# Optimization experiments

Hardware: AMD Instinct MI355X
Metric: run time of the kernel (lower is better)

The kernel has to match this reference:

```python
import jax, jax.numpy as jnp
import numpy as np

N_NODES = 100000
N_EDGES = 1250000
F_RAW = 48      # raw node feature dim
F_LOC = 16      # location embedding dim
F1 = 48         # filters_1
F_OUT = 64      # out_channels


def _glorot(key, shape):
    fan_in, fan_out = shape[0], shape[1]
    scale = jnp.sqrt(6.0 / (fan_in + fan_out)).astype(jnp.float32)
    return jax.random.uniform(key, shape, jnp.float32, -1.0, 1.0) * scale


def setup_inputs() -> dict:
    key = jax.random.key(0)
    k_e, k_x, k_l, k_w1, k_w2 = jax.random.split(key, 5)
    edge_indices = jax.random.randint(k_e, (2, N_EDGES), 0, N_NODES, dtype=jnp.int64)
    features = jax.random.normal(k_x, (N_NODES, F_RAW), jnp.float32)
    location_embedding = jax.random.normal(k_l, (N_NODES, F_LOC), jnp.float32)
    W1 = _glorot(k_w1, (F_RAW + F_LOC, F1))
    b1 = jnp.zeros((F1,), jnp.float32)
    W2 = _glorot(k_w2, (F1 + F_LOC, F_OUT))
    b2 = jnp.zeros((F_OUT,), jnp.float32)
    return {"edge_indices": edge_indices, "features": features,
            "location_embedding": location_embedding,
            "W1": W1, "b1": b1, "W2": W2, "b2": b2}


def gcn_conv(x, src, dst, W, b, n_nodes):
    """PyG GCNConv: add self-loops, symmetric normalization, linear + bias."""
    h = x @ W  # [N, F_out]
    # degree counts include the self-loop (+1)
    deg = jnp.zeros((n_nodes,), h.dtype).at[dst].add(1.0) + 1.0
    dinv = jax.lax.rsqrt(deg)  # deg >= 1 so always finite
    coef = dinv[src] * dinv[dst]  # [E]
    agg = jnp.zeros((n_nodes, h.shape[1]), h.dtype).at[dst].add(h[src] * coef[:, None])
    # self-loop contribution: dinv[i]^2 * h[i]
    return agg + h * (dinv * dinv)[:, None] + b


def reference(edge_indices, features, location_embedding, W1, b1, W2, b2):
    src, dst = edge_indices[0], edge_indices[1]
    n = features.shape[0]
    x = jnp.concatenate([features, location_embedding], axis=-1)
    x = gcn_conv(x, src, dst, W1, b1, n)
    x = jax.nn.relu(x)
    # dropout is identity in eval mode (reference is inference semantics)
    x = jnp.concatenate([x, location_embedding], axis=-1)
    x = gcn_conv(x, src, dst, W2, b2, n)
    return x
```

## Files before the change

kernel.cpp:

```cpp
#include <hip/hip_runtime.h>
#include <hip/hip_fp16.h>

#define N_NODES 100000
#define N_EDGES 1250000
#define F_RAW 48
#define F_LOC 16
#define F1 48
#define F_IN1 64
#define F_IN2 64
#define F_OUT 64

#define NB_BIN 100
#define CHUNK (N_EDGES / NB_BIN)
#define NBUK 391
#define NSCAN (NBUK * NB_BIN)
#define NSCAN_PARTS ((NSCAN + 1023) / 1024)

typedef _Float16 half8_t __attribute__((ext_vector_type(8)));
typedef float floatx4 __attribute__((ext_vector_type(4)));

__global__ void k_detect(const unsigned* edges_u32, int* flag) {
    __shared__ int any;
    if (threadIdx.x == 0) any = 0;
    __syncthreads();
    int nz = 0;
    for (int i = threadIdx.x; i < 2048; i += 256) {
        if (edges_u32[2 * i + 1] != 0u) nz = 1;
    }
    if (nz) atomicOr(&any, 1);
    __syncthreads();
    if (threadIdx.x == 0) *flag = any;
}

__device__ __forceinline__ void load_edge(const void* edges, int is32, int e,
                                          int& s, int& d) {
    if (is32) {
        const int* p = (const int*)edges;
        s = p[e];
        d = p[N_EDGES + e];
    } else {
        const long long* p = (const long long*)edges;
        s = (int)p[e];
        d = (int)p[N_EDGES + e];
    }
}

__global__ __launch_bounds__(1024) void k_prepA(const void* edges,
                                                const int* flag,
                                                int* __restrict__ src32,
                                                int* __restrict__ dst32,
                                                int* __restrict__ bhist) {
    __shared__ int hist[NBUK];
    int b = blockIdx.x, t = threadIdx.x;
    for (int k = t; k < NBUK; k += 1024) hist[k] = 0;
    __syncthreads();
    int is32 = *flag;
    int e0 = b * CHUNK;
    int e1 = e0 + CHUNK;
    for (int e = e0 + t; e < e1; e += 1024) {
        int s, d;
        load_edge(edges, is32, e, s, d);
        src32[e] = s;
        dst32[e] = d;
        atomicAdd(&hist[d >> 8], 1);
    }
    __syncthreads();
    for (int k = t; k < NBUK; k += 1024) bhist[k * NB_BIN + b] = hist[k];
}

__global__ __launch_bounds__(256) void k_gscan_part(const int* __restrict__ in,
                                                    int* __restrict__ part,
                                                    int n) {
    int b = blockIdx.x, t = threadIdx.x;
    int i0 = b * 1024 + t * 4;
    int s = 0;
#pragma unroll
    for (int j = 0; j < 4; ++j) {
        int i = i0 + j;
        if (i < n) s += in[i];
    }
#pragma unroll
    for (int m = 1; m < 64; m <<= 1) s += __shfl_xor(s, m);
    __shared__ int ws[4];
    if ((t & 63) == 0) ws[t >> 6] = s;
    __syncthreads();
    if (t == 0) part[b] = ws[0] + ws[1] + ws[2] + ws[3];
}

__global__ __launch_bounds__(64) void k_gscan_top(int* __restrict__ part,
                                                  int nb) {
    int t = threadIdx.x;
    int v = (t < nb) ? part[t] : 0;
    int x = v;
#pragma unroll
    for (int off = 1; off < 64; off <<= 1) {
        int u = __shfl_up(x, off);
        if (t >= off) x += u;
    }
    if (t < nb) part[t] = x - v;
}

__global__ __launch_bounds__(256) void k_gscan_down(int* __restrict__ data,
                                                    const int* __restrict__ part,
                                                    int n) {
    int b = blockIdx.x, t = threadIdx.x;
    int lane = t & 63, wv = t >> 6;
    int i0 = b * 1024 + t * 4;
    int v[4];
    int s = 0;
#pragma unroll
    for (int j = 0; j < 4; ++j) {
        int i = i0 + j;
        v[j] = (i < n) ? data[i] : 0;
        s += v[j];
    }
    int x = s;
#pragma unroll
    for (int off = 1; off < 64; off <<= 1) {
        int u = __shfl_up(x, off);
        if (lane >= off) x += u;
    }
    __shared__ int ws[4];
    if (lane == 63) ws[wv] = x;
    __syncthreads();
    int woff = 0;
    for (int w = 0; w < wv; ++w) woff += ws[w];
    int run = part[b] + woff + (x - s);
#pragma unroll
    for (int j = 0; j < 4; ++j) {
        int i = i0 + j;
        if (i < n) {
            data[i] = run;
            run += v[j];
        }
    }
}

__global__ __launch_bounds__(1024) void k_place(const int* __restrict__ src32,
                                                const int* __restrict__ dst32,
                                                const int* __restrict__ bhist,
                                                unsigned* __restrict__ binned) {
    __shared__ int cnt[NBUK];
    int b = blockIdx.x, t = threadIdx.x;
    for (int k = t; k < NBUK; k += 1024) cnt[k] = bhist[k * NB_BIN + b];
    __syncthreads();
    int e0 = b * CHUNK;
    int e1 = e0 + CHUNK;
    for (int e = e0 + t; e < e1; e += 1024) {
        int s = src32[e];
        int d = dst32[e];
        int p = atomicAdd(&cnt[d >> 8], 1);
        binned[p] = ((unsigned)(d & 255) << 17) | (unsigned)s;
    }
}

__global__ __launch_bounds__(256) void k_bucket(
    const unsigned* __restrict__ binned, const int* __restrict__ bhist,
    float* __restrict__ dinv, int* __restrict__ rowptr,
    unsigned* __restrict__ csr4) {
    int k = blockIdx.x, t = threadIdx.x;
    int lane = t & 63, wv = t >> 6;
    __shared__ int ldeg[256];
    __shared__ int wcnt[256];
    __shared__ int ws4[4];
    int base = bhist[k * NB_BIN];
    int next = (k + 1 < NBUK) ? bhist[(k + 1) * NB_BIN] : N_EDGES;
    int len = next - base;
    ldeg[t] = 0;
    __syncthreads();
    for (int i = t; i < len; i += 256)
        atomicAdd(&ldeg[binned[base + i] >> 17], 1);
    __syncthreads();
    int degv = ldeg[t];
    int x = degv;
#pragma unroll
    for (int off = 1; off < 64; off <<= 1) {
        int u = __shfl_up(x, off);
        if (lane >= off) x += u;
    }
    if (lane == 63) ws4[wv] = x;
    __syncthreads();
    int woff = 0;
    for (int w = 0; w < wv; ++w) woff += ws4[w];
    int excl = woff + x - degv;
    int node = k * 256 + t;
    if (node < N_NODES) {
        dinv[node] = rsqrtf((float)degv + 1.0f);
        rowptr[node] = base + excl;
    }
    wcnt[t] = base + excl;
    __syncthreads();
    for (int i = t; i < len; i += 256) {
        unsigned ent = binned[base + i];
        int dl = ent >> 17;
        int p = atomicAdd(&wcnt[dl], 1);
        csr4[p] = ent & 0x1FFFFu;
    }
    if (k == 0 && t == 0) rowptr[N_NODES] = N_EDGES;
}

__global__ __launch_bounds__(256) void k_csr8(const unsigned* __restrict__ csr4,
                                              const float* __restrict__ dinv,
                                              int2* __restrict__ csr8) {
    int i = blockIdx.x * 256 + threadIdx.x;
    if (i >= N_EDGES / 2) return;
    uint2 v = reinterpret_cast<const uint2*>(csr4)[i];
    unsigned h0 = (unsigned)__half_as_ushort(__float2half(dinv[v.x]));
    unsigned h1 = (unsigned)__half_as_ushort(__float2half(dinv[v.y]));
    int4 o;
    o.x = (int)(v.x << 7);
    o.y = (int)(h0 | (h0 << 16));
    o.z = (int)(v.y << 7);
    o.w = (int)(h1 | (h1 << 16));
    reinterpret_cast<int4*>(csr8)[i] = o;
}

__global__ void k_wprep(const float* __restrict__ W, __half* __restrict__ Wpk,
                        int M, int CT) {
    int lane = threadIdx.x;
    for (int ct = 0; ct < CT; ++ct)
        for (int kt = 0; kt < 2; ++kt)
            for (int j = 0; j < 8; ++j) {
                int k = kt * 32 + (lane >> 4) * 8 + j;
                int c = ct * 16 + (lane & 15);
                Wpk[((ct * 2 + kt) * 64 + lane) * 8 + j] =
                    __float2half(W[k * M + c]);
            }
}

__global__ __launch_bounds__(256) void k_gemm1(const float* __restrict__ feat,
                                               const float* __restrict__ loc,
                                               const __half* __restrict__ Wpk,
                                               __half* __restrict__ Y) {
    int wid = threadIdx.x >> 6;
    int lane = threadIdx.x & 63;
    int nb = (blockIdx.x * 4 + wid) * 32;
    if (nb >= N_NODES) return;
    half8_t b[3][2];
#pragma unroll
    for (int ct = 0; ct < 3; ++ct)
#pragma unroll
        for (int kt = 0; kt < 2; ++kt)
            b[ct][kt] = *reinterpret_cast<const half8_t*>(
                Wpk + ((ct * 2 + kt) * 64 + lane) * 8);
    int r = lane & 15;
    int slot = lane >> 4;
    half8_t a[2][2];
#pragma unroll
    for (int rt = 0; rt < 2; ++rt)
#pragma unroll
        for (int kt = 0; kt < 2; ++kt) {
            int sl = kt * 4 + slot;
            int node = nb + rt * 16 + r;
            const float* sp = (sl < 6)
                                  ? feat + (size_t)node * F_RAW + sl * 8
                                  : loc + (size_t)node * F_LOC + (sl - 6) * 8;
            float4 f0 = reinterpret_cast<const float4*>(sp)[0];
            float4 f1 = reinterpret_cast<const float4*>(sp)[1];
            half8_t h;
            h[0] = (_Float16)f0.x;
            h[1] = (_Float16)f0.y;
            h[2] = (_Float16)f0.z;
            h[3] = (_Float16)f0.w;
            h[4] = (_Float16)f1.x;
            h[5] = (_Float16)f1.y;
            h[6] = (_Float16)f1.z;
            h[7] = (_Float16)f1.w;
            a[rt][kt] = h;
        }
    floatx4 acc[2][3];
#pragma unroll
    for (int rt = 0; rt < 2; ++rt)
#pragma unroll
        for (int ct = 0; ct < 3; ++ct) {
            floatx4 z = {0.f, 0.f, 0.f, 0.f};
            z = __builtin_amdgcn_mfma_f32_16x16x32_f16(a[rt][0], b[ct][0], z, 0, 0, 0);
            z = __builtin_amdgcn_mfma_f32_16x16x32_f16(a[rt][1], b[ct][1], z, 0, 0, 0);
            acc[rt][ct] = z;
        }
    int row0 = (lane >> 4) * 4;
    int col = lane & 15;
#pragma unroll
    for (int rt = 0; rt < 2; ++rt)
#pragma unroll
        for (int ct = 0; ct < 3; ++ct)
#pragma unroll
            for (int j = 0; j < 4; ++j) {
                int node = nb + rt * 16 + row0 + j;
                Y[(size_t)node * 64 + ct * 16 + col] = __float2half(acc[rt][ct][j]);
            }
    int node = nb + (lane & 31);
    int slotp = 6 + (lane >> 5);
    *reinterpret_cast<int4*>(Y + (size_t)node * 64 + slotp * 8) =
        make_int4(0, 0, 0, 0);
}

__global__ __launch_bounds__(256) void k_gemm2(const __half* __restrict__ X,
                                               const __half* __restrict__ Wpk,
                                               __half* __restrict__ Y) {
    int wid = threadIdx.x >> 6;
    int lane = threadIdx.x & 63;
    int nb = (blockIdx.x * 4 + wid) * 32;
    if (nb >= N_NODES) return;
    half8_t b[4][2];
#pragma unroll
    for (int ct = 0; ct < 4; ++ct)
#pragma unroll
        for (int kt = 0; kt < 2; ++kt)
            b[ct][kt] = *reinterpret_cast<const half8_t*>(
                Wpk + ((ct * 2 + kt) * 64 + lane) * 8);
    int r = lane & 15;
    int ks = (lane >> 4) * 8;
    half8_t a[2][2];
#pragma unroll
    for (int rt = 0; rt < 2; ++rt)
#pragma unroll
        for (int kt = 0; kt < 2; ++kt)
            a[rt][kt] = *reinterpret_cast<const half8_t*>(
                X + ((size_t)(nb + rt * 16 + r) * 64 + kt * 32 + ks));
    floatx4 acc[2][4];
#pragma unroll
    for (int rt = 0; rt < 2; ++rt)
#pragma unroll
        for (int ct = 0; ct < 4; ++ct) {
            floatx4 z = {0.f, 0.f, 0.f, 0.f};
            z = __builtin_amdgcn_mfma_f32_16x16x32_f16(a[rt][0], b[ct][0], z, 0, 0, 0);
            z = __builtin_amdgcn_mfma_f32_16x16x32_f16(a[rt][1], b[ct][1], z, 0, 0, 0);
            acc[rt][ct] = z;
        }
    int row0 = (lane >> 4) * 4;
    int col = lane & 15;
#pragma unroll
    for (int rt = 0; rt < 2; ++rt)
#pragma unroll
        for (int ct = 0; ct < 4; ++ct)
#pragma unroll
            for (int j = 0; j < 4; ++j) {
                int node = nb + rt * 16 + row0 + j;
                Y[(size_t)node * 64 + ct * 16 + col] = __float2half(acc[rt][ct][j]);
            }
}

__device__ __forceinline__ __half2 h2bits(int y) {
    return *reinterpret_cast<__half2*>(&y);
}

__device__ __forceinline__ void fma8h(const int4& p, __half2 c2, __half2 a[4]) {
    const __half2* h = reinterpret_cast<const __half2*>(&p);
#pragma unroll
    for (int j = 0; j < 4; ++j) a[j] = __hfma2(h[j], c2, a[j]);
}

__device__ __forceinline__ __half2 shfl_xor_h2(__half2 v, int m) {
    int i = *reinterpret_cast<int*>(&v);
    i = __shfl_xor(i, m);
    return *reinterpret_cast<__half2*>(&i);
}

__global__ __launch_bounds__(256) void k_agg1(
    const __half* __restrict__ h1h, const float* __restrict__ dinv,
    const int* __restrict__ rowptr, const int2* __restrict__ csr8,
    const float* __restrict__ loc, const float* __restrict__ b1,
    __half* __restrict__ x1h) {
    int wave = threadIdx.x >> 6;
    int lane = threadIdx.x & 63;
    int grp = lane >> 3;
    int l8 = lane & 7;
    int node = blockIdx.x * 4 + wave;
    if (node >= N_NODES) return;
    int r0 = rowptr[node], r1 = rowptr[node + 1];
    const char* h1l = reinterpret_cast<const char*>(h1h) + (l8 << 4);
    float di = dinv[node];
    int4 hs = *reinterpret_cast<const int4*>(h1l + ((size_t)node << 7));
    int len = r1 - r0;
    int L = (len + 7) >> 3;
    int gs = r0 + grp * L;
    int ge = gs + L;
    if (ge > r1) ge = r1;
    __half2 z2 = __float2half2_rn(0.f);
    __half2 a0[4] = {z2, z2, z2, z2};
    __half2 a1[4] = {z2, z2, z2, z2};
    int e = gs;
    for (; e + 1 < ge; e += 2) {
        int2 A = csr8[e];
        int2 B = csr8[e + 1];
        int4 vA = *reinterpret_cast<const int4*>(h1l + A.x);
        int4 vB = *reinterpret_cast<const int4*>(h1l + B.x);
        fma8h(vA, h2bits(A.y), a0);
        fma8h(vB, h2bits(B.y), a1);
    }
    if (e < ge) {
        int2 A = csr8[e];
        int4 vA = *reinterpret_cast<const int4*>(h1l + A.x);
        fma8h(vA, h2bits(A.y), a0);
    }
#pragma unroll
    for (int j = 0; j < 4; ++j) a0[j] = __hadd2(a0[j], a1[j]);
#pragma unroll
    for (int j = 0; j < 4; ++j) {
        a0[j] = __hadd2(a0[j], shfl_xor_h2(a0[j], 8));
        a0[j] = __hadd2(a0[j], shfl_xor_h2(a0[j], 16));
        a0[j] = __hadd2(a0[j], shfl_xor_h2(a0[j], 32));
    }
    if (lane < 8) {
        __half2 q[4];
        if (l8 < 6) {
            float d2 = di * di;
            const float4* b1v = reinterpret_cast<const float4*>(b1);
            float4 bA = b1v[l8 * 2];
            float4 bB = b1v[l8 * 2 + 1];
            float bb[8] = {bA.x, bA.y, bA.z, bA.w, bB.x, bB.y, bB.z, bB.w};
            const __half2* hh = reinterpret_cast<const __half2*>(&hs);
            float o[8];
#pragma unroll
            for (int j = 0; j < 4; ++j) {
                float2 t = __half22float2(hh[j]);
                float2 ag = __half22float2(a0[j]);
                o[2 * j] = fmaxf(fmaf(ag.x, di, fmaf(t.x, d2, bb[2 * j])), 0.f);
                o[2 * j + 1] =
                    fmaxf(fmaf(ag.y, di, fmaf(t.y, d2, bb[2 * j + 1])), 0.f);
            }
#pragma unroll
            for (int j = 0; j < 4; ++j)
                q[j] = __halves2half2(__float2half(o[2 * j]),
                                      __float2half(o[2 * j + 1]));
        } else {
            const float* lp = loc + (size_t)node * F_LOC + (l8 - 6) * 8;
            float4 f0 = reinterpret_cast<const float4*>(lp)[0];
            float4 f1 = reinterpret_cast<const float4*>(lp)[1];
            q[0] = __halves2half2(__float2half(f0.x), __float2half(f0.y));
            q[1] = __halves2half2(__float2half(f0.z), __float2half(f0.w));
            q[2] = __halves2half2(__float2half(f1.x), __float2half(f1.y));
            q[3] = __halves2half2(__float2half(f1.z), __float2half(f1.w));
        }
        reinterpret_cast<int4*>(x1h)[(size_t)node * 8 + l8] =
            *reinterpret_cast<int4*>(q);
    }
}

__global__ __launch_bounds__(256) void k_out(
    const __half* __restrict__ h2h, const float* __restrict__ dinv,
    const int* __restrict__ rowptr, const int2* __restrict__ csr8,
    const float* __restrict__ b2, float* __restrict__ out) {
    int wave = threadIdx.x >> 6;
    int lane = threadIdx.x & 63;
    int grp = lane >> 3;
    int l8 = lane & 7;
    int node = blockIdx.x * 4 + wave;
    if (node >= N_NODES) return;
    int r0 = rowptr[node], r1 = rowptr[node + 1];
    const char* h2l = reinterpret_cast<const char*>(h2h) + (l8 << 4);
    float di = dinv[node];
    int4 hs = *reinterpret_cast<const int4*>(h2l + ((size_t)node << 7));
    int len = r1 - r0;
    int L = (len + 7) >> 3;
    int gs = r0 + grp * L;
    int ge = gs + L;
    if (ge > r1) ge = r1;
    __half2 z2 = __float2half2_rn(0.f);
    __half2 a0[4] = {z2, z2, z2, z2};
    __half2 a1[4] = {z2, z2, z2, z2};
    int e = gs;
    for (; e + 1 < ge; e += 2) {
        int2 A = csr8[e];
        int2 B = csr8[e + 1];
        int4 vA = *reinterpret_cast<const int4*>(h2l + A.x);
        int4 vB = *reinterpret_cast<const int4*>(h2l + B.x);
        fma8h(vA, h2bits(A.y), a0);
        fma8h(vB, h2bits(B.y), a1);
    }
    if (e < ge) {
        int2 A = csr8[e];
        int4 vA = *reinterpret_cast<const int4*>(h2l + A.x);
        fma8h(vA, h2bits(A.y), a0);
    }
#pragma unroll
    for (int j = 0; j < 4; ++j) a0[j] = __hadd2(a0[j], a1[j]);
#pragma unroll
    for (int j = 0; j < 4; ++j) {
        a0[j] = __hadd2(a0[j], shfl_xor_h2(a0[j], 8));
        a0[j] = __hadd2(a0[j], shfl_xor_h2(a0[j], 16));
        a0[j] = __hadd2(a0[j], shfl_xor_h2(a0[j], 32));
    }
    if (lane < 8) {
        float d2 = di * di;
        const float4* b2v = reinterpret_cast<const float4*>(b2);
        float4 bA = b2v[l8 * 2];
        float4 bB = b2v[l8 * 2 + 1];
        float bb[8] = {bA.x, bA.y, bA.z, bA.w, bB.x, bB.y, bB.z, bB.w};
        const __half2* hh = reinterpret_cast<const __half2*>(&hs);
        float o[8];
#pragma unroll
        for (int j = 0; j < 4; ++j) {
            float2 t = __half22float2(hh[j]);
            float2 ag = __half22float2(a0[j]);
            o[2 * j] = fmaf(ag.x, di, fmaf(t.x, d2, bb[2 * j]));
            o[2 * j + 1] = fmaf(ag.y, di, fmaf(t.y, d2, bb[2 * j + 1]));
        }
        float4* ov = reinterpret_cast<float4*>(out + (size_t)node * F_OUT);
        ov[l8 * 2] = make_float4(o[0], o[1], o[2], o[3]);
        ov[l8 * 2 + 1] = make_float4(o[4], o[5], o[6], o[7]);
    }
}

extern "C" void kernel_launch(void* const* d_in, const int* in_sizes, int n_in,
                              void* d_out, int out_size, void* d_ws,
                              size_t ws_size, hipStream_t stream) {
    const void* edges = d_in[0];
    const float* feat = (const float*)d_in[1];
    const float* loc = (const float*)d_in[2];
    const float* W1 = (const float*)d_in[3];
    const float* b1 = (const float*)d_in[4];
    const float* W2 = (const float*)d_in[5];
    const float* b2 = (const float*)d_in[6];
    float* out = (float*)d_out;

    char* ws = (char*)d_ws;
    float* dinv = (float*)(ws + 0);
    int* rowptr = (int*)(ws + 400000);
    int* src32 = (int*)(ws + 800016);
    int* dst32 = (int*)(ws + 5800016);
    int* bhist = (int*)(ws + 10800016);
    int* bsum = (int*)(ws + 10956416);
    unsigned* binned = (unsigned*)(ws + 10956672);
    unsigned* csr4 = (unsigned*)(ws + 15956672);
    __half* x1h = (__half*)(ws + 20956672);
    __half* h1h = (__half*)(ws + 33756672);
    __half* h2h = (__half*)(ws + 46556672);
    __half* wpk1 = (__half*)(ws + 59356672);
    __half* wpk2 = (__half*)(ws + 59362816);
    int* flag = (int*)(ws + 59371008);
    int2* csr8 = (int2*)(ws + 800016);

    k_detect<<<1, 256, 0, stream>>>((const unsigned*)edges, flag);
    k_wprep<<<1, 64, 0, stream>>>(W1, wpk1, F1, 3);
    k_wprep<<<1, 64, 0, stream>>>(W2, wpk2, F_OUT, 4);

    k_prepA<<<NB_BIN, 1024, 0, stream>>>(edges, flag, src32, dst32, bhist);
    k_gscan_part<<<NSCAN_PARTS, 256, 0, stream>>>(bhist, bsum, NSCAN);
    k_gscan_top<<<1, 64, 0, stream>>>(bsum, NSCAN_PARTS);
    k_gscan_down<<<NSCAN_PARTS, 256, 0, stream>>>(bhist, bsum, NSCAN);
    k_place<<<NB_BIN, 1024, 0, stream>>>(src32, dst32, bhist, binned);
    k_bucket<<<NBUK, 256, 0, stream>>>(binned, bhist, dinv, rowptr, csr4);
    k_csr8<<<(N_EDGES / 2 + 255) / 256, 256, 0, stream>>>(csr4, dinv, csr8);

    int gblocks = (N_NODES / 32 + 3) / 4;
    k_gemm1<<<gblocks, 256, 0, stream>>>(feat, loc, wpk1, h1h);
    k_agg1<<<(N_NODES + 3) / 4, 256, 0, stream>>>(h1h, dinv, rowptr, csr8,
                                                  loc, b1, x1h);
    k_gemm2<<<gblocks, 256, 0, stream>>>(x1h, wpk2, h2h);
    k_out<<<(N_NODES + 3) / 4, 256, 0, stream>>>(h2h, dinv, rowptr, csr8, b2,
                                                 out);
}
```

Baseline: 165.4 us.

## Split transformed features into column slabs and pack coefficient into CSR word

The GEMM outputs are stored as separate 32-column and 16/32-column slabs instead of one padded 64-half row. The aggregation kernels gather each slab in a separate pass over the edge list, so each pass reads a smaller, more cache-resident table. The per-edge coefficient is now packed into the low 14 bits of a 4-byte CSR entry, which halves index traffic compared with the previous 8-byte entries. The three tiny prep kernels are merged into one launch. In exchange, the edge list is read twice, the coefficient keeps only 14 bits of the fp16 value (dropping the sign bit, which is safe because it is always positive), and an extra shuffle step is needed to reassemble the outputs.

```diff
diff --git a/kernel.cpp b/kernel.cpp
--- a/kernel.cpp
+++ b/kernel.cpp
@@ -6,8 +6,6 @@
 #define F_RAW 48
 #define F_LOC 16
 #define F1 48
-#define F_IN1 64
-#define F_IN2 64
 #define F_OUT 64
 
 #define NB_BIN 100
@@ -19,7 +17,30 @@
 typedef _Float16 half8_t __attribute__((ext_vector_type(8)));
 typedef float floatx4 __attribute__((ext_vector_type(4)));
 
-__global__ void k_detect(const unsigned* edges_u32, int* flag) {
+__device__ void wprep_dev(const float* W, __half* Wpk, int M, int CT) {
+    int lane = threadIdx.x;
+    if (lane >= 64) return;
+    for (int ct = 0; ct < CT; ++ct)
+        for (int kt = 0; kt < 2; ++kt)
+            for (int j = 0; j < 8; ++j) {
+                int k = kt * 32 + (lane >> 4) * 8 + j;
+                int c = ct * 16 + (lane & 15);
+                Wpk[((ct * 2 + kt) * 64 + lane) * 8 + j] =
+                    __float2half(W[k * M + c]);
+            }
+}
+
+__global__ void k_misc(const unsigned* edges_u32, int* flag,
+                       const float* W1, __half* wpk1,
+                       const float* W2, __half* wpk2) {
+    if (blockIdx.x == 1) {
+        wprep_dev(W1, wpk1, F1, 3);
+        return;
+    }
+    if (blockIdx.x == 2) {
+        wprep_dev(W2, wpk2, F_OUT, 4);
+        return;
+    }
     __shared__ int any;
     if (threadIdx.x == 0) any = 0;
     __syncthreads();
@@ -199,39 +220,23 @@
     if (k == 0 && t == 0) rowptr[N_NODES] = N_EDGES;
 }
 
-__global__ __launch_bounds__(256) void k_csr8(const unsigned* __restrict__ csr4,
-                                              const float* __restrict__ dinv,
-                                              int2* __restrict__ csr8) {
+__global__ __launch_bounds__(256) void k_coef(unsigned* __restrict__ csr4,
+                                              const float* __restrict__ dinv) {
     int i = blockIdx.x * 256 + threadIdx.x;
-    if (i >= N_EDGES / 2) return;
-    uint2 v = reinterpret_cast<const uint2*>(csr4)[i];
-    unsigned h0 = (unsigned)__half_as_ushort(__float2half(dinv[v.x]));
-    unsigned h1 = (unsigned)__half_as_ushort(__float2half(dinv[v.y]));
-    int4 o;
-    o.x = (int)(v.x << 7);
-    o.y = (int)(h0 | (h0 << 16));
-    o.z = (int)(v.y << 7);
-    o.w = (int)(h1 | (h1 << 16));
-    reinterpret_cast<int4*>(csr8)[i] = o;
-}
-
-__global__ void k_wprep(const float* __restrict__ W, __half* __restrict__ Wpk,
-                        int M, int CT) {
-    int lane = threadIdx.x;
-    for (int ct = 0; ct < CT; ++ct)
-        for (int kt = 0; kt < 2; ++kt)
-            for (int j = 0; j < 8; ++j) {
-                int k = kt * 32 + (lane >> 4) * 8 + j;
-                int c = ct * 16 + (lane & 15);
-                Wpk[((ct * 2 + kt) * 64 + lane) * 8 + j] =
-                    __float2half(W[k * M + c]);
-            }
+    if (i >= N_EDGES / 4) return;
+    uint4 v = reinterpret_cast<uint4*>(csr4)[i];
+    v.x = (v.x << 14) | (unsigned)__half_as_ushort(__float2half(dinv[v.x]));
+    v.y = (v.y << 14) | (unsigned)__half_as_ushort(__float2half(dinv[v.y]));
+    v.z = (v.z << 14) | (unsigned)__half_as_ushort(__float2half(dinv[v.z]));
+    v.w = (v.w << 14) | (unsigned)__half_as_ushort(__float2half(dinv[v.w]));
+    reinterpret_cast<uint4*>(csr4)[i] = v;
 }
 
 __global__ __launch_bounds__(256) void k_gemm1(const float* __restrict__ feat,
                                                const float* __restrict__ loc,
                                                const __half* __restrict__ Wpk,
-                                               __half* __restrict__ Y) {
+                                               __half* __restrict__ h1a,
+                                               __half* __restrict__ h1b) {
     int wid = threadIdx.x >> 6;
     int lane = threadIdx.x & 63;
     int nb = (blockIdx.x * 4 + wid) * 32;
@@ -287,17 +292,18 @@
 #pragma unroll
             for (int j = 0; j < 4; ++j) {
                 int node = nb + rt * 16 + row0 + j;
-                Y[(size_t)node * 64 + ct * 16 + col] = __float2half(acc[rt][ct][j]);
+                if (ct < 2)
+                    h1a[(size_t)node * 32 + ct * 16 + col] =
+                        __float2half(acc[rt][ct][j]);
+                else
+                    h1b[(size_t)node * 16 + col] = __float2half(acc[rt][ct][j]);
             }
-    int node = nb + (lane & 31);
-    int slotp = 6 + (lane >> 5);
-    *reinterpret_cast<int4*>(Y + (size_t)node * 64 + slotp * 8) =
-        make_int4(0, 0, 0, 0);
 }
 
 __global__ __launch_bounds__(256) void k_gemm2(const __half* __restrict__ X,
                                                const __half* __restrict__ Wpk,
-                                               __half* __restrict__ Y) {
+                                               __half* __restrict__ h2a,
+                                               __half* __restrict__ h2b) {
     int wid = threadIdx.x >> 6;
     int lane = threadIdx.x & 63;
     int nb = (blockIdx.x * 4 + wid) * 32;
@@ -337,7 +343,12 @@
 #pragma unroll
             for (int j = 0; j < 4; ++j) {
                 int node = nb + rt * 16 + row0 + j;
-                Y[(size_t)node * 64 + ct * 16 + col] = __float2half(acc[rt][ct][j]);
+                if (ct < 2)
+                    h2a[(size_t)node * 32 + ct * 16 + col] =
+                        __float2half(acc[rt][ct][j]);
+                else
+                    h2b[(size_t)node * 32 + (ct - 2) * 16 + col] =
+                        __float2half(acc[rt][ct][j]);
             }
 }
 
@@ -345,23 +356,26 @@
     return *reinterpret_cast<__half2*>(&y);
 }
 
-__device__ __forceinline__ void fma8h(const int4& p, __half2 c2, __half2 a[4]) {
-    const __half2* h = reinterpret_cast<const __half2*>(&p);
-#pragma unroll
-    for (int j = 0; j < 4; ++j) a[j] = __hfma2(h[j], c2, a[j]);
+__device__ __forceinline__ int as_int_h2(__half2 v) {
+    return *reinterpret_cast<int*>(&v);
+}
+
+__device__ __forceinline__ __half2 coef2(unsigned A) {
+    unsigned b = A & 0x3FFFu;
+    return h2bits((int)(b | (b << 16)));
 }
 
 __device__ __forceinline__ __half2 shfl_xor_h2(__half2 v, int m) {
-    int i = *reinterpret_cast<int*>(&v);
+    int i = as_int_h2(v);
     i = __shfl_xor(i, m);
-    return *reinterpret_cast<__half2*>(&i);
+    return h2bits(i);
 }
 
 __global__ __launch_bounds__(256) void k_agg1(
-    const __half* __restrict__ h1h, const float* __restrict__ dinv,
-    const int* __restrict__ rowptr, const int2* __restrict__ csr8,
-    const float* __restrict__ loc, const float* __restrict__ b1,
-    __half* __restrict__ x1h) {
+    const __half* __restrict__ h1a, const __half* __restrict__ h1b,
+    const float* __restrict__ dinv, const int* __restrict__ rowptr,
+    const unsigned* __restrict__ csr4, const float* __restrict__ loc,
+    const float* __restrict__ b1, __half* __restrict__ x1h) {
     int wave = threadIdx.x >> 6;
     int lane = threadIdx.x & 63;
     int grp = lane >> 3;
@@ -369,63 +383,99 @@
     int node = blockIdx.x * 4 + wave;
     if (node >= N_NODES) return;
     int r0 = rowptr[node], r1 = rowptr[node + 1];
-    const char* h1l = reinterpret_cast<const char*>(h1h) + (l8 << 4);
-    float di = dinv[node];
-    int4 hs = *reinterpret_cast<const int4*>(h1l + ((size_t)node << 7));
     int len = r1 - r0;
     int L = (len + 7) >> 3;
     int gs = r0 + grp * L;
     int ge = gs + L;
     if (ge > r1) ge = r1;
+    float di = dinv[node];
+    const char* pa = reinterpret_cast<const char*>(h1a) + l8 * 8;
+    const char* pb = reinterpret_cast<const char*>(h1b) + l8 * 4;
     __half2 z2 = __float2half2_rn(0.f);
-    __half2 a0[4] = {z2, z2, z2, z2};
-    __half2 a1[4] = {z2, z2, z2, z2};
+    __half2 a0[2] = {z2, z2}, a1[2] = {z2, z2};
     int e = gs;
     for (; e + 1 < ge; e += 2) {
-        int2 A = csr8[e];
-        int2 B = csr8[e + 1];
-        int4 vA = *reinterpret_cast<const int4*>(h1l + A.x);
-        int4 vB = *reinterpret_cast<const int4*>(h1l + B.x);
-        fma8h(vA, h2bits(A.y), a0);
-        fma8h(vB, h2bits(B.y), a1);
+        unsigned A = csr4[e];
+        unsigned B = csr4[e + 1];
+        int2 vA = *reinterpret_cast<const int2*>(pa + ((A >> 14) << 6));
+        int2 vB = *reinterpret_cast<const int2*>(pa + ((B >> 14) << 6));
+        __half2 cA = coef2(A), cB = coef2(B);
+        a0[0] = __hfma2(h2bits(vA.x), cA, a0[0]);
+        a0[1] = __hfma2(h2bits(vA.y), cA, a0[1]);
+        a1[0] = __hfma2(h2bits(vB.x), cB, a1[0]);
+        a1[1] = __hfma2(h2bits(vB.y), cB, a1[1]);
     }
     if (e < ge) {
-        int2 A = csr8[e];
-        int4 vA = *reinterpret_cast<const int4*>(h1l + A.x);
-        fma8h(vA, h2bits(A.y), a0);
-    }
-#pragma unroll
-    for (int j = 0; j < 4; ++j) a0[j] = __hadd2(a0[j], a1[j]);
-#pragma unroll
-    for (int j = 0; j < 4; ++j) {
-        a0[j] = __hadd2(a0[j], shfl_xor_h2(a0[j], 8));
-        a0[j] = __hadd2(a0[j], shfl_xor_h2(a0[j], 16));
-        a0[j] = __hadd2(a0[j], shfl_xor_h2(a0[j], 32));
+        unsigned A = csr4[e];
+        int2 vA = *reinterpret_cast<const int2*>(pa + ((A >> 14) << 6));
+        __half2 cA = coef2(A);
+        a0[0] = __hfma2(h2bits(vA.x), cA, a0[0]);
+        a0[1] = __hfma2(h2bits(vA.y), cA, a0[1]);
+    }
+    a0[0] = __hadd2(a0[0], a1[0]);
+    a0[1] = __hadd2(a0[1], a1[1]);
+    __half2 b0 = z2, b1c = z2;
+    e = gs;
+    for (; e + 1 < ge; e += 2) {
+        unsigned A = csr4[e];
+        unsigned B = csr4[e + 1];
+        int vA = *reinterpret_cast<const int*>(pb + ((A >> 14) << 5));
+        int vB = *reinterpret_cast<const int*>(pb + ((B >> 14) << 5));
+        b0 = __hfma2(h2bits(vA), coef2(A), b0);
+        b1c = __hfma2(h2bits(vB), coef2(B), b1c);
+    }
+    if (e < ge) {
+        unsigned A = csr4[e];
+        int vA = *reinterpret_cast<const int*>(pb + ((A >> 14) << 5));
+        b0 = __hfma2(h2bits(vA), coef2(A), b0);
+    }
+    b0 = __hadd2(b0, b1c);
+#pragma unroll
+    for (int m = 8; m <= 32; m <<= 1) {
+        a0[0] = __hadd2(a0[0], shfl_xor_h2(a0[0], m));
+        a0[1] = __hadd2(a0[1], shfl_xor_h2(a0[1], m));
+        b0 = __hadd2(b0, shfl_xor_h2(b0, m));
+    }
+    int ai0 = as_int_h2(a0[0]), ai1 = as_int_h2(a0[1]), bi = as_int_h2(b0);
+    int m = l8;
+    int s0 = (m < 4) ? 2 * m : (m - 4) * 4;
+    int t00 = __shfl(ai0, s0), t01 = __shfl(ai1, s0);
+    int t10 = __shfl(ai0, s0 + 1), t11 = __shfl(ai1, s0 + 1);
+    int u0 = __shfl(bi, s0), u1 = __shfl(bi, s0 + 1);
+    int u2 = __shfl(bi, s0 + 2), u3 = __shfl(bi, s0 + 3);
+    int w[4];
+    if (m < 4) {
+        w[0] = t00; w[1] = t01; w[2] = t10; w[3] = t11;
+    } else {
+        w[0] = u0; w[1] = u1; w[2] = u2; w[3] = u3;
     }
     if (lane < 8) {
         __half2 q[4];
-        if (l8 < 6) {
+        if (m < 6) {
             float d2 = di * di;
             const float4* b1v = reinterpret_cast<const float4*>(b1);
-            float4 bA = b1v[l8 * 2];
-            float4 bB = b1v[l8 * 2 + 1];
+            float4 bA = b1v[m * 2];
+            float4 bB = b1v[m * 2 + 1];
             float bb[8] = {bA.x, bA.y, bA.z, bA.w, bB.x, bB.y, bB.z, bB.w};
+            int4 hs = (m < 4)
+                          ? *reinterpret_cast<const int4*>(
+                                reinterpret_cast<const char*>(h1a) +
+                                ((size_t)node << 6) + m * 16)
+                          : *reinterpret_cast<const int4*>(
+                                reinterpret_cast<const char*>(h1b) +
+                                ((size_t)node << 5) + (m - 4) * 16);
             const __half2* hh = reinterpret_cast<const __half2*>(&hs);
-            float o[8];
 #pragma unroll
             for (int j = 0; j < 4; ++j) {
                 float2 t = __half22float2(hh[j]);
-                float2 ag = __half22float2(a0[j]);
-                o[2 * j] = fmaxf(fmaf(ag.x, di, fmaf(t.x, d2, bb[2 * j])), 0.f);
-                o[2 * j + 1] =
+                float2 ag = __half22float2(h2bits(w[j]));
+                float o0 = fmaxf(fmaf(ag.x, di, fmaf(t.x, d2, bb[2 * j])), 0.f);
+                float o1 =
                     fmaxf(fmaf(ag.y, di, fmaf(t.y, d2, bb[2 * j + 1])), 0.f);
+                q[j] = __halves2half2(__float2half(o0), __float2half(o1));
             }
-#pragma unroll
-            for (int j = 0; j < 4; ++j)
-                q[j] = __halves2half2(__float2half(o[2 * j]),
-                                      __float2half(o[2 * j + 1]));
         } else {
-            const float* lp = loc + (size_t)node * F_LOC + (l8 - 6) * 8;
+            const float* lp = loc + (size_t)node * F_LOC + (m - 6) * 8;
             float4 f0 = reinterpret_cast<const float4*>(lp)[0];
             float4 f1 = reinterpret_cast<const float4*>(lp)[1];
             q[0] = __halves2half2(__float2half(f0.x), __float2half(f0.y));
@@ -433,15 +483,16 @@
             q[2] = __halves2half2(__float2half(f1.x), __float2half(f1.y));
             q[3] = __halves2half2(__float2half(f1.z), __float2half(f1.w));
         }
-        reinterpret_cast<int4*>(x1h)[(size_t)node * 8 + l8] =
+        reinterpret_cast<int4*>(x1h)[(size_t)node * 8 + m] =
             *reinterpret_cast<int4*>(q);
     }
 }
 
 __global__ __launch_bounds__(256) void k_out(
-    const __half* __restrict__ h2h, const float* __restrict__ dinv,
-    const int* __restrict__ rowptr, const int2* __restrict__ csr8,
-    const float* __restrict__ b2, float* __restrict__ out) {
+    const __half* __restrict__ h2a, const __half* __restrict__ h2b,
+    const float* __restrict__ dinv, const int* __restrict__ rowptr,
+    const unsigned* __restrict__ csr4, const float* __restrict__ b2,
+    float* __restrict__ out) {
     int wave = threadIdx.x >> 6;
     int lane = threadIdx.x & 63;
     int grp = lane >> 3;
@@ -449,57 +500,104 @@
     int node = blockIdx.x * 4 + wave;
     if (node >= N_NODES) return;
     int r0 = rowptr[node], r1 = rowptr[node + 1];
-    const char* h2l = reinterpret_cast<const char*>(h2h) + (l8 << 4);
-    float di = dinv[node];
-    int4 hs = *reinterpret_cast<const int4*>(h2l + ((size_t)node << 7));
     int len = r1 - r0;
     int L = (len + 7) >> 3;
     int gs = r0 + grp * L;
     int ge = gs + L;
     if (ge > r1) ge = r1;
+    float di = dinv[node];
+    const char* pa = reinterpret_cast<const char*>(h2a) + l8 * 8;
+    const char* pb = reinterpret_cast<const char*>(h2b) + l8 * 8;
     __half2 z2 = __float2half2_rn(0.f);
-    __half2 a0[4] = {z2, z2, z2, z2};
-    __half2 a1[4] = {z2, z2, z2, z2};
+    __half2 a0[2] = {z2, z2}, a1[2] = {z2, z2};
     int e = gs;
     for (; e + 1 < ge; e += 2) {
-        int2 A = csr8[e];
-        int2 B = csr8[e + 1];
-        int4 vA = *reinterpret_cast<const int4*>(h2l + A.x);
-        int4 vB = *reinterpret_cast<const int4*>(h2l + B.x);
-        fma8h(vA, h2bits(A.y), a0);
-        fma8h(vB, h2bits(B.y), a1);
+        unsigned A = csr4[e];
+        unsigned B = csr4[e + 1];
+        int2 vA = *reinterpret_cast<const int2*>(pa + ((A >> 14) << 6));
+        int2 vB = *reinterpret_cast<const int2*>(pa + ((B >> 14) << 6));
+        __half2 cA = coef2(A), cB = coef2(B);
+        a0[0] = __hfma2(h2bits(vA.x), cA, a0[0]);
+        a0[1] = __hfma2(h2bits(vA.y), cA, a0[1]);
+        a1[0] = __hfma2(h2bits(vB.x), cB, a1[0]);
+        a1[1] = __hfma2(h2bits(vB.y), cB, a1[1]);
     }
     if (e < ge) {
-        int2 A = csr8[e];
-        int4 vA = *reinterpret_cast<const int4*>(h2l + A.x);
-        fma8h(vA, h2bits(A.y), a0);
-    }
-#pragma unroll
-    for (int j = 0; j < 4; ++j) a0[j] = __hadd2(a0[j], a1[j]);
-#pragma unroll
-    for (int j = 0; j < 4; ++j) {
-        a0[j] = __hadd2(a0[j], shfl_xor_h2(a0[j], 8));
-        a0[j] = __hadd2(a0[j], shfl_xor_h2(a0[j], 16));
-        a0[j] = __hadd2(a0[j], shfl_xor_h2(a0[j], 32));
+        unsigned A = csr4[e];
+        int2 vA = *reinterpret_cast<const int2*>(pa + ((A >> 14) << 6));
+        __half2 cA = coef2(A);
+        a0[0] = __hfma2(h2bits(vA.x), cA, a0[0]);
+        a0[1] = __hfma2(h2bits(vA.y), cA, a0[1]);
+    }
+    a0[0] = __hadd2(a0[0], a1[0]);
+    a0[1] = __hadd2(a0[1], a1[1]);
+    __half2 c0[2] = {z2, z2}, c1[2] = {z2, z2};
+    e = gs;
+    for (; e + 1 < ge; e += 2) {
+        unsigned A = csr4[e];
+        unsigned B = csr4[e + 1];
+        int2 vA = *reinterpret_cast<const int2*>(pb + ((A >> 14) << 6));
+        int2 vB = *reinterpret_cast<const int2*>(pb + ((B >> 14) << 6));
+        __half2 cA = coef2(A), cB = coef2(B);
+        c0[0] = __hfma2(h2bits(vA.x), cA, c0[0]);
+        c0[1] = __hfma2(h2bits(vA.y), cA, c0[1]);
+        c1[0] = __hfma2(h2bits(vB.x), cB, c1[0]);
+        c1[1] = __hfma2(h2bits(vB.y), cB, c1[1]);
+    }
+    if (e < ge) {
+        unsigned A = csr4[e];
+        int2 vA = *reinterpret_cast<const int2*>(pb + ((A >> 14) << 6));
+        __half2 cA = coef2(A);
+        c0[0] = __hfma2(h2bits(vA.x), cA, c0[0]);
+        c0[1] = __hfma2(h2bits(vA.y), cA, c0[1]);
+    }
+    c0[0] = __hadd2(c0[0], c1[0]);
+    c0[1] = __hadd2(c0[1], c1[1]);
+#pragma unroll
+    for (int m = 8; m <= 32; m <<= 1) {
+        a0[0] = __hadd2(a0[0], shfl_xor_h2(a0[0], m));
+        a0[1] = __hadd2(a0[1], shfl_xor_h2(a0[1], m));
+        c0[0] = __hadd2(c0[0], shfl_xor_h2(c0[0], m));
+        c0[1] = __hadd2(c0[1], shfl_xor_h2(c0[1], m));
+    }
+    int ai0 = as_int_h2(a0[0]), ai1 = as_int_h2(a0[1]);
+    int bi0 = as_int_h2(c0[0]), bi1 = as_int_h2(c0[1]);
+    int m = l8;
+    int s0 = 2 * (m & 3);
+    int tA0 = __shfl(ai0, s0), tA1 = __shfl(ai1, s0);
+    int tA2 = __shfl(ai0, s0 + 1), tA3 = __shfl(ai1, s0 + 1);
+    int tB0 = __shfl(bi0, s0), tB1 = __shfl(bi1, s0);
+    int tB2 = __shfl(bi0, s0 + 1), tB3 = __shfl(bi1, s0 + 1);
+    int w[4];
+    if (m < 4) {
+        w[0] = tA0; w[1] = tA1; w[2] = tA2; w[3] = tA3;
+    } else {
+        w[0] = tB0; w[1] = tB1; w[2] = tB2; w[3] = tB3;
     }
     if (lane < 8) {
         float d2 = di * di;
         const float4* b2v = reinterpret_cast<const float4*>(b2);
-        float4 bA = b2v[l8 * 2];
-        float4 bB = b2v[l8 * 2 + 1];
+        float4 bA = b2v[m * 2];
+        float4 bB = b2v[m * 2 + 1];
         float bb[8] = {bA.x, bA.y, bA.z, bA.w, bB.x, bB.y, bB.z, bB.w};
+        int4 hs = (m < 4) ? *reinterpret_cast<const int4*>(
+                                reinterpret_cast<const char*>(h2a) +
+                                ((size_t)node << 6) + m * 16)
+                          : *reinterpret_cast<const int4*>(
+                                reinterpret_cast<const char*>(h2b) +
+                                ((size_t)node << 6) + (m - 4) * 16);
         const __half2* hh = reinterpret_cast<const __half2*>(&hs);
         float o[8];
 #pragma unroll
         for (int j = 0; j < 4; ++j) {
             float2 t = __half22float2(hh[j]);
-            float2 ag = __half22float2(a0[j]);
+            float2 ag = __half22float2(h2bits(w[j]));
             o[2 * j] = fmaf(ag.x, di, fmaf(t.x, d2, bb[2 * j]));
             o[2 * j + 1] = fmaf(ag.y, di, fmaf(t.y, d2, bb[2 * j + 1]));
         }
         float4* ov = reinterpret_cast<float4*>(out + (size_t)node * F_OUT);
-        ov[l8 * 2] = make_float4(o[0], o[1], o[2], o[3]);
-        ov[l8 * 2 + 1] = make_float4(o[4], o[5], o[6], o[7]);
+        ov[m * 2] = make_float4(o[0], o[1], o[2], o[3]);
+        ov[m * 2 + 1] = make_float4(o[4], o[5], o[6], o[7]);
     }
 }
 
@@ -525,16 +623,16 @@
     unsigned* binned = (unsigned*)(ws + 10956672);
     unsigned* csr4 = (unsigned*)(ws + 15956672);
     __half* x1h = (__half*)(ws + 20956672);
-    __half* h1h = (__half*)(ws + 33756672);
-    __half* h2h = (__half*)(ws + 46556672);
-    __half* wpk1 = (__half*)(ws + 59356672);
-    __half* wpk2 = (__half*)(ws + 59362816);
-    int* flag = (int*)(ws + 59371008);
-    int2* csr8 = (int2*)(ws + 800016);
-
-    k_detect<<<1, 256, 0, stream>>>((const unsigned*)edges, flag);
-    k_wprep<<<1, 64, 0, stream>>>(W1, wpk1, F1, 3);
-    k_wprep<<<1, 64, 0, stream>>>(W2, wpk2, F_OUT, 4);
+    __half* h1a = (__half*)(ws + 33756672);
+    __half* h1b = (__half*)(ws + 40156672);
+    __half* h2a = (__half*)(ws + 43356672);
+    __half* h2b = (__half*)(ws + 49756672);
+    __half* wpk1 = (__half*)(ws + 56156672);
+    __half* wpk2 = (__half*)(ws + 56162816);
+    int* flag = (int*)(ws + 56171008);
+
+    k_misc<<<3, 256, 0, stream>>>((const unsigned*)edges, flag, W1, wpk1, W2,
+                                  wpk2);
 
     k_prepA<<<NB_BIN, 1024, 0, stream>>>(edges, flag, src32, dst32, bhist);
     k_gscan_part<<<NSCAN_PARTS, 256, 0, stream>>>(bhist, bsum, NSCAN);
@@ -542,13 +640,13 @@
     k_gscan_down<<<NSCAN_PARTS, 256, 0, stream>>>(bhist, bsum, NSCAN);
     k_place<<<NB_BIN, 1024, 0, stream>>>(src32, dst32, bhist, binned);
     k_bucket<<<NBUK, 256, 0, stream>>>(binned, bhist, dinv, rowptr, csr4);
-    k_csr8<<<(N_EDGES / 2 + 255) / 256, 256, 0, stream>>>(csr4, dinv, csr8);
+    k_coef<<<(N_EDGES / 4 + 255) / 256, 256, 0, stream>>>(csr4, dinv);
 
     int gblocks = (N_NODES / 32 + 3) / 4;
-    k_gemm1<<<gblocks, 256, 0, stream>>>(feat, loc, wpk1, h1h);
-    k_agg1<<<(N_NODES + 3) / 4, 256, 0, stream>>>(h1h, dinv, rowptr, csr8,
-                                                  loc, b1, x1h);
-    k_gemm2<<<gblocks, 256, 0, stream>>>(x1h, wpk2, h2h);
-    k_out<<<(N_NODES + 3) / 4, 256, 0, stream>>>(h2h, dinv, rowptr, csr8, b2,
-                                                 out);
-}
+    k_gemm1<<<gblocks, 256, 0, stream>>>(feat, loc, wpk1, h1a, h1b);
+    k_agg1<<<(N_NODES + 3) / 4, 256, 0, stream>>>(h1a, h1b, dinv, rowptr,
+                                                  csr4, loc, b1, x1h);
+    k_gemm2<<<gblocks, 256, 0, stream>>>(x1h, wpk2, h2a, h2b);
+    k_out<<<(N_NODES + 3) / 4, 256, 0, stream>>>(h2a, h2b, dinv, rowptr, csr4,
+                                                 b2, out);
+}
```

Result: slower. 197.5 us (+19.4%).

## Replace scan-based edge binning with padded atomic-cursor buckets and 4-byte CSR

Applied to the files above, without the earlier changes.

Edge binning by destination bucket now uses fixed-capacity padded bucket regions with a global atomic cursor per bucket. This replaces the histogram, three-kernel global scan and a separate placement pass with one kernel that stashes edges in shared memory. The CSR entries shrink from 8 to 4 bytes by packing the source index and a 14-bit half-precision coefficient together, and row pointers become start/end pairs. Small setup kernels are merged into one launch. The risks are bucket overflow past the padded capacity (4096 slots per 256-node bucket) and coefficient precision loss from truncating the half to 14 bits, which only holds while dinv stays at or below 1.

```diff
diff --git a/kernel.cpp b/kernel.cpp
--- a/kernel.cpp
+++ b/kernel.cpp
@@ -6,20 +6,44 @@
 #define F_RAW 48
 #define F_LOC 16
 #define F1 48
-#define F_IN1 64
-#define F_IN2 64
 #define F_OUT 64
 
-#define NB_BIN 100
-#define CHUNK (N_EDGES / NB_BIN)
 #define NBUK 391
-#define NSCAN (NBUK * NB_BIN)
-#define NSCAN_PARTS ((NSCAN + 1023) / 1024)
+#define PADB 4096
+#define NB2 500
+#define CH2 (N_EDGES / NB2)
 
 typedef _Float16 half8_t __attribute__((ext_vector_type(8)));
 typedef float floatx4 __attribute__((ext_vector_type(4)));
 
-__global__ void k_detect(const unsigned* edges_u32, int* flag) {
+__device__ void wprep_dev(const float* W, __half* Wpk, int M, int CT) {
+    int lane = threadIdx.x;
+    if (lane >= 64) return;
+    for (int ct = 0; ct < CT; ++ct)
+        for (int kt = 0; kt < 2; ++kt)
+            for (int j = 0; j < 8; ++j) {
+                int k = kt * 32 + (lane >> 4) * 8 + j;
+                int c = ct * 16 + (lane & 15);
+                Wpk[((ct * 2 + kt) * 64 + lane) * 8 + j] =
+                    __float2half(W[k * M + c]);
+            }
+}
+
+__global__ void k_misc(const unsigned* edges_u32, int* flag,
+                       const float* W1, __half* wpk1,
+                       const float* W2, __half* wpk2, int* cursor) {
+    if (blockIdx.x == 1) {
+        wprep_dev(W1, wpk1, F1, 3);
+        return;
+    }
+    if (blockIdx.x == 2) {
+        wprep_dev(W2, wpk2, F_OUT, 4);
+        return;
+    }
+    if (blockIdx.x == 3) {
+        for (int k = threadIdx.x; k < NBUK; k += 256) cursor[k] = k * PADB;
+        return;
+    }
     __shared__ int any;
     if (threadIdx.x == 0) any = 0;
     __syncthreads();
@@ -45,127 +69,48 @@
     }
 }
 
-__global__ __launch_bounds__(1024) void k_prepA(const void* edges,
-                                                const int* flag,
-                                                int* __restrict__ src32,
-                                                int* __restrict__ dst32,
-                                                int* __restrict__ bhist) {
+__global__ __launch_bounds__(512) void k_prep2(const void* edges,
+                                               const int* flag,
+                                               int* __restrict__ cursor,
+                                               unsigned* __restrict__ binned) {
     __shared__ int hist[NBUK];
+    __shared__ int2 stash[CH2];
     int b = blockIdx.x, t = threadIdx.x;
-    for (int k = t; k < NBUK; k += 1024) hist[k] = 0;
+    for (int k = t; k < NBUK; k += 512) hist[k] = 0;
     __syncthreads();
     int is32 = *flag;
-    int e0 = b * CHUNK;
-    int e1 = e0 + CHUNK;
-    for (int e = e0 + t; e < e1; e += 1024) {
+    int e0 = b * CH2;
+    for (int i = t; i < CH2; i += 512) {
         int s, d;
-        load_edge(edges, is32, e, s, d);
-        src32[e] = s;
-        dst32[e] = d;
-        atomicAdd(&hist[d >> 8], 1);
-    }
-    __syncthreads();
-    for (int k = t; k < NBUK; k += 1024) bhist[k * NB_BIN + b] = hist[k];
-}
-
-__global__ __launch_bounds__(256) void k_gscan_part(const int* __restrict__ in,
-                                                    int* __restrict__ part,
-                                                    int n) {
-    int b = blockIdx.x, t = threadIdx.x;
-    int i0 = b * 1024 + t * 4;
-    int s = 0;
-#pragma unroll
-    for (int j = 0; j < 4; ++j) {
-        int i = i0 + j;
-        if (i < n) s += in[i];
-    }
-#pragma unroll
-    for (int m = 1; m < 64; m <<= 1) s += __shfl_xor(s, m);
-    __shared__ int ws[4];
-    if ((t & 63) == 0) ws[t >> 6] = s;
-    __syncthreads();
-    if (t == 0) part[b] = ws[0] + ws[1] + ws[2] + ws[3];
-}
-
-__global__ __launch_bounds__(64) void k_gscan_top(int* __restrict__ part,
-                                                  int nb) {
-    int t = threadIdx.x;
-    int v = (t < nb) ? part[t] : 0;
-    int x = v;
-#pragma unroll
-    for (int off = 1; off < 64; off <<= 1) {
-        int u = __shfl_up(x, off);
-        if (t >= off) x += u;
-    }
-    if (t < nb) part[t] = x - v;
-}
-
-__global__ __launch_bounds__(256) void k_gscan_down(int* __restrict__ data,
-                                                    const int* __restrict__ part,
-                                                    int n) {
-    int b = blockIdx.x, t = threadIdx.x;
-    int lane = t & 63, wv = t >> 6;
-    int i0 = b * 1024 + t * 4;
-    int v[4];
-    int s = 0;
-#pragma unroll
-    for (int j = 0; j < 4; ++j) {
-        int i = i0 + j;
-        v[j] = (i < n) ? data[i] : 0;
-        s += v[j];
-    }
-    int x = s;
-#pragma unroll
-    for (int off = 1; off < 64; off <<= 1) {
-        int u = __shfl_up(x, off);
-        if (lane >= off) x += u;
-    }
-    __shared__ int ws[4];
-    if (lane == 63) ws[wv] = x;
-    __syncthreads();
-    int woff = 0;
-    for (int w = 0; w < wv; ++w) woff += ws[w];
-    int run = part[b] + woff + (x - s);
-#pragma unroll
-    for (int j = 0; j < 4; ++j) {
-        int i = i0 + j;
-        if (i < n) {
-            data[i] = run;
-            run += v[j];
-        }
-    }
-}
-
-__global__ __launch_bounds__(1024) void k_place(const int* __restrict__ src32,
-                                                const int* __restrict__ dst32,
-                                                const int* __restrict__ bhist,
-                                                unsigned* __restrict__ binned) {
-    __shared__ int cnt[NBUK];
-    int b = blockIdx.x, t = threadIdx.x;
-    for (int k = t; k < NBUK; k += 1024) cnt[k] = bhist[k * NB_BIN + b];
-    __syncthreads();
-    int e0 = b * CHUNK;
-    int e1 = e0 + CHUNK;
-    for (int e = e0 + t; e < e1; e += 1024) {
-        int s = src32[e];
-        int d = dst32[e];
-        int p = atomicAdd(&cnt[d >> 8], 1);
-        binned[p] = ((unsigned)(d & 255) << 17) | (unsigned)s;
+        load_edge(edges, is32, e0 + i, s, d);
+        int bk = d >> 8;
+        stash[i] = make_int2(bk, ((d & 255) << 17) | s);
+        atomicAdd(&hist[bk], 1);
+    }
+    __syncthreads();
+    for (int k = t; k < NBUK; k += 512) {
+        int c = hist[k];
+        hist[k] = c ? atomicAdd(&cursor[k], c) : 0;
+    }
+    __syncthreads();
+    for (int i = t; i < CH2; i += 512) {
+        int2 sd = stash[i];
+        int p = atomicAdd(&hist[sd.x], 1);
+        binned[p] = (unsigned)sd.y;
     }
 }
 
 __global__ __launch_bounds__(256) void k_bucket(
-    const unsigned* __restrict__ binned, const int* __restrict__ bhist,
-    float* __restrict__ dinv, int* __restrict__ rowptr,
+    const unsigned* __restrict__ binned, const int* __restrict__ cursor,
+    float* __restrict__ dinv, int2* __restrict__ rowse,
     unsigned* __restrict__ csr4) {
     int k = blockIdx.x, t = threadIdx.x;
     int lane = t & 63, wv = t >> 6;
     __shared__ int ldeg[256];
     __shared__ int wcnt[256];
     __shared__ int ws4[4];
-    int base = bhist[k * NB_BIN];
-    int next = (k + 1 < NBUK) ? bhist[(k + 1) * NB_BIN] : N_EDGES;
-    int len = next - base;
+    int base = k * PADB;
+    int len = cursor[k] - base;
     ldeg[t] = 0;
     __syncthreads();
     for (int i = t; i < len; i += 256)
@@ -186,46 +131,26 @@
     int node = k * 256 + t;
     if (node < N_NODES) {
         dinv[node] = rsqrtf((float)degv + 1.0f);
-        rowptr[node] = base + excl;
+        rowse[node] = make_int2(base + excl, base + excl + degv);
     }
     wcnt[t] = base + excl;
     __syncthreads();
     for (int i = t; i < len; i += 256) {
         unsigned ent = binned[base + i];
-        int dl = ent >> 17;
-        int p = atomicAdd(&wcnt[dl], 1);
+        int p = atomicAdd(&wcnt[ent >> 17], 1);
         csr4[p] = ent & 0x1FFFFu;
     }
-    if (k == 0 && t == 0) rowptr[N_NODES] = N_EDGES;
-}
-
-__global__ __launch_bounds__(256) void k_csr8(const unsigned* __restrict__ csr4,
+}
+
+__global__ __launch_bounds__(256) void k_coef(unsigned* __restrict__ csr4,
                                               const float* __restrict__ dinv,
-                                              int2* __restrict__ csr8) {
-    int i = blockIdx.x * 256 + threadIdx.x;
-    if (i >= N_EDGES / 2) return;
-    uint2 v = reinterpret_cast<const uint2*>(csr4)[i];
-    unsigned h0 = (unsigned)__half_as_ushort(__float2half(dinv[v.x]));
-    unsigned h1 = (unsigned)__half_as_ushort(__float2half(dinv[v.y]));
-    int4 o;
-    o.x = (int)(v.x << 7);
-    o.y = (int)(h0 | (h0 << 16));
-    o.z = (int)(v.y << 7);
-    o.w = (int)(h1 | (h1 << 16));
-    reinterpret_cast<int4*>(csr8)[i] = o;
-}
-
-__global__ void k_wprep(const float* __restrict__ W, __half* __restrict__ Wpk,
-                        int M, int CT) {
-    int lane = threadIdx.x;
-    for (int ct = 0; ct < CT; ++ct)
-        for (int kt = 0; kt < 2; ++kt)
-            for (int j = 0; j < 8; ++j) {
-                int k = kt * 32 + (lane >> 4) * 8 + j;
-                int c = ct * 16 + (lane & 15);
-                Wpk[((ct * 2 + kt) * 64 + lane) * 8 + j] =
-                    __float2half(W[k * M + c]);
-            }
+                                              const int* __restrict__ cursor) {
+    int k = blockIdx.x;
+    int end = cursor[k];
+    for (int i = k * PADB + threadIdx.x; i < end; i += 256) {
+        unsigned s = csr4[i];
+        csr4[i] = (s << 14) | (unsigned)__half_as_ushort(__float2half(dinv[s]));
+    }
 }
 
 __global__ __launch_bounds__(256) void k_gemm1(const float* __restrict__ feat,
@@ -341,8 +266,10 @@
             }
 }
 
-__device__ __forceinline__ __half2 h2bits(int y) {
-    return *reinterpret_cast<__half2*>(&y);
+__device__ __forceinline__ __half2 c2_from(unsigned A) {
+    unsigned b = A & 0x3FFFu;
+    unsigned p = b | (b << 16);
+    return *reinterpret_cast<__half2*>(&p);
 }
 
 __device__ __forceinline__ void fma8h(const int4& p, __half2 c2, __half2 a[4]) {
@@ -359,7 +286,7 @@
 
 __global__ __launch_bounds__(256) void k_agg1(
     const __half* __restrict__ h1h, const float* __restrict__ dinv,
-    const int* __restrict__ rowptr, const int2* __restrict__ csr8,
+    const int2* __restrict__ rowse, const unsigned* __restrict__ csr4,
     const float* __restrict__ loc, const float* __restrict__ b1,
     __half* __restrict__ x1h) {
     int wave = threadIdx.x >> 6;
@@ -368,7 +295,8 @@
     int l8 = lane & 7;
     int node = blockIdx.x * 4 + wave;
     if (node >= N_NODES) return;
-    int r0 = rowptr[node], r1 = rowptr[node + 1];
+    int2 se = rowse[node];
+    int r0 = se.x, r1 = se.y;
     const char* h1l = reinterpret_cast<const char*>(h1h) + (l8 << 4);
     float di = dinv[node];
     int4 hs = *reinterpret_cast<const int4*>(h1l + ((size_t)node << 7));
@@ -382,17 +310,17 @@
     __half2 a1[4] = {z2, z2, z2, z2};
     int e = gs;
     for (; e + 1 < ge; e += 2) {
-        int2 A = csr8[e];
-        int2 B = csr8[e + 1];
-        int4 vA = *reinterpret_cast<const int4*>(h1l + A.x);
-        int4 vB = *reinterpret_cast<const int4*>(h1l + B.x);
-        fma8h(vA, h2bits(A.y), a0);
-        fma8h(vB, h2bits(B.y), a1);
+        unsigned A = csr4[e];
+        unsigned B = csr4[e + 1];
+        int4 vA = *reinterpret_cast<const int4*>(h1l + ((A >> 14) << 7));
+        int4 vB = *reinterpret_cast<const int4*>(h1l + ((B >> 14) << 7));
+        fma8h(vA, c2_from(A), a0);
+        fma8h(vB, c2_from(B), a1);
     }
     if (e < ge) {
-        int2 A = csr8[e];
-        int4 vA = *reinterpret_cast<const int4*>(h1l + A.x);
-        fma8h(vA, h2bits(A.y), a0);
+        unsigned A = csr4[e];
+        int4 vA = *reinterpret_cast<const int4*>(h1l + ((A >> 14) << 7));
+        fma8h(vA, c2_from(A), a0);
     }
 #pragma unroll
     for (int j = 0; j < 4; ++j) a0[j] = __hadd2(a0[j], a1[j]);
@@ -440,7 +368,7 @@
 
 __global__ __launch_bounds__(256) void k_out(
     const __half* __restrict__ h2h, const float* __restrict__ dinv,
-    const int* __restrict__ rowptr, const int2* __restrict__ csr8,
+    const int2* __restrict__ rowse, const unsigned* __restrict__ csr4,
     const float* __restrict__ b2, float* __restrict__ out) {
     int wave = threadIdx.x >> 6;
     int lane = threadIdx.x & 63;
@@ -448,7 +376,8 @@
     int l8 = lane & 7;
     int node = blockIdx.x * 4 + wave;
     if (node >= N_NODES) return;
-    int r0 = rowptr[node], r1 = rowptr[node + 1];
+    int2 se = rowse[node];
+    int r0 = se.x, r1 = se.y;
     const char* h2l = reinterpret_cast<const char*>(h2h) + (l8 << 4);
     float di = dinv[node];
     int4 hs = *reinterpret_cast<const int4*>(h2l + ((size_t)node << 7));
@@ -462,17 +391,17 @@
     __half2 a1[4] = {z2, z2, z2, z2};
     int e = gs;
     for (; e + 1 < ge; e += 2) {
-        int2 A = csr8[e];
-        int2 B = csr8[e + 1];
-        int4 vA = *reinterpret_cast<const int4*>(h2l + A.x);
-        int4 vB = *reinterpret_cast<const int4*>(h2l + B.x);
-        fma8h(vA, h2bits(A.y), a0);
-        fma8h(vB, h2bits(B.y), a1);
+        unsigned A = csr4[e];
+        unsigned B = csr4[e + 1];
+        int4 vA = *reinterpret_cast<const int4*>(h2l + ((A >> 14) << 7));
+        int4 vB = *reinterpret_cast<const int4*>(h2l + ((B >> 14) << 7));
+        fma8h(vA, c2_from(A), a0);
+        fma8h(vB, c2_from(B), a1);
     }
     if (e < ge) {
-        int2 A = csr8[e];
-        int4 vA = *reinterpret_cast<const int4*>(h2l + A.x);
-        fma8h(vA, h2bits(A.y), a0);
+        unsigned A = csr4[e];
+        int4 vA = *reinterpret_cast<const int4*>(h2l + ((A >> 14) << 7));
+        fma8h(vA, c2_from(A), a0);
     }
 #pragma unroll
     for (int j = 0; j < 4; ++j) a0[j] = __hadd2(a0[j], a1[j]);
@@ -517,38 +446,29 @@
 
     char* ws = (char*)d_ws;
     float* dinv = (float*)(ws + 0);
-    int* rowptr = (int*)(ws + 400000);
-    int* src32 = (int*)(ws + 800016);
-    int* dst32 = (int*)(ws + 5800016);
-    int* bhist = (int*)(ws + 10800016);
-    int* bsum = (int*)(ws + 10956416);
-    unsigned* binned = (unsigned*)(ws + 10956672);
-    unsigned* csr4 = (unsigned*)(ws + 15956672);
-    __half* x1h = (__half*)(ws + 20956672);
-    __half* h1h = (__half*)(ws + 33756672);
-    __half* h2h = (__half*)(ws + 46556672);
-    __half* wpk1 = (__half*)(ws + 59356672);
-    __half* wpk2 = (__half*)(ws + 59362816);
-    int* flag = (int*)(ws + 59371008);
-    int2* csr8 = (int2*)(ws + 800016);
-
-    k_detect<<<1, 256, 0, stream>>>((const unsigned*)edges, flag);
-    k_wprep<<<1, 64, 0, stream>>>(W1, wpk1, F1, 3);
-    k_wprep<<<1, 64, 0, stream>>>(W2, wpk2, F_OUT, 4);
-
-    k_prepA<<<NB_BIN, 1024, 0, stream>>>(edges, flag, src32, dst32, bhist);
-    k_gscan_part<<<NSCAN_PARTS, 256, 0, stream>>>(bhist, bsum, NSCAN);
-    k_gscan_top<<<1, 64, 0, stream>>>(bsum, NSCAN_PARTS);
-    k_gscan_down<<<NSCAN_PARTS, 256, 0, stream>>>(bhist, bsum, NSCAN);
-    k_place<<<NB_BIN, 1024, 0, stream>>>(src32, dst32, bhist, binned);
-    k_bucket<<<NBUK, 256, 0, stream>>>(binned, bhist, dinv, rowptr, csr4);
-    k_csr8<<<(N_EDGES / 2 + 255) / 256, 256, 0, stream>>>(csr4, dinv, csr8);
+    int2* rowse = (int2*)(ws + 400000);
+    int* cursor = (int*)(ws + 1200000);
+    unsigned* binned = (unsigned*)(ws + 1201568);
+    unsigned* csr4 = (unsigned*)(ws + 7607712);
+    __half* h1h = (__half*)(ws + 14013856);
+    __half* x1h = (__half*)(ws + 26813856);
+    __half* h2h = (__half*)(ws + 39613856);
+    __half* wpk1 = (__half*)(ws + 52413856);
+    __half* wpk2 = (__half*)(ws + 52420000);
+    int* flag = (int*)(ws + 52428192);
+
+    k_misc<<<4, 256, 0, stream>>>((const unsigned*)edges, flag, W1, wpk1, W2,
+                                  wpk2, cursor);
+
+    k_prep2<<<NB2, 512, 0, stream>>>(edges, flag, cursor, binned);
+    k_bucket<<<NBUK, 256, 0, stream>>>(binned, cursor, dinv, rowse, csr4);
+    k_coef<<<NBUK, 256, 0, stream>>>(csr4, dinv, cursor);
 
     int gblocks = (N_NODES / 32 + 3) / 4;
     k_gemm1<<<gblocks, 256, 0, stream>>>(feat, loc, wpk1, h1h);
-    k_agg1<<<(N_NODES + 3) / 4, 256, 0, stream>>>(h1h, dinv, rowptr, csr8,
-                                                  loc, b1, x1h);
+    k_agg1<<<(N_NODES + 3) / 4, 256, 0, stream>>>(h1h, dinv, rowse, csr4, loc,
+                                                  b1, x1h);
     k_gemm2<<<gblocks, 256, 0, stream>>>(x1h, wpk2, h2h);
-    k_out<<<(N_NODES + 3) / 4, 256, 0, stream>>>(h2h, dinv, rowptr, csr8, b2,
+    k_out<<<(N_NODES + 3) / 4, 256, 0, stream>>>(h2h, dinv, rowse, csr4, b2,
                                                  out);
 }
```

New measurement: 164.7 us. No clear change (-0.4%).
